# Kernel optimization log

Measured on AMD Instinct MI355X. Metric: run time of the kernel, lower is better.

## Reference

```python
import jax, jax.numpy as jnp
import numpy as np

NUM_BINS = 64


def _centers_width(num_bins):
    edges = np.linspace(-0.05, 1.05, num_bins + 1)
    delta = edges[2] - edges[1]
    centers = (edges + delta / 2)[:-1]
    return jnp.asarray(centers, jnp.float32), jnp.float32(delta / 2)

_CENTERS, _WIDTH = _centers_width(NUM_BINS)

_YUV = jnp.asarray([[0.299, 0.587, 0.114],
                    [-0.14713, -0.28886, 0.436],
                    [0.615, -0.51499, -0.10001]], jnp.float32)


def _soft_hist(img):
    # img: [B, C, H, W]; scale from [-1,1] -> [0,1] as in extract_hist
    img = (img + 1.0) * 0.5
    # bin_centers_conv (w=1, b=-center) -> x - c ; abs ; bin_widths_conv (w=-1, b=width) -> width - |x-c|
    d = jnp.abs(img[:, :, None, :, :] - _CENTERS[None, None, :, None, None])  # [B,C,bins,H,W]
    act = jnp.float32(1.01) ** (_WIDTH - d)
    act = jnp.where(act > 1.0, act, 0.0)  # nn.Threshold(1, 0)
    return act.mean(axis=(3, 4))  # AdaptiveAvgPool2d(1) -> [B, C, bins]


def _to_yuv(x):
    return jnp.einsum('ij,bjhw->bihw', _YUV, x)


def _emd(h1, h2):
    # per channel: mean over batch of sum over bins of cumsum diff; summed over channels
    diff = jnp.cumsum(h1, axis=-1) - jnp.cumsum(h2, axis=-1)  # [B,C,bins]
    return diff.sum(axis=-1).mean(axis=0).sum()


def setup_inputs() -> dict:
    key = jax.random.key(0)
    k1, k2 = jax.random.split(key)
    shape = (8, 3, 256, 256)
    return {
        'input_img': jax.random.normal(k1, shape, dtype=jnp.float32),
        'reference_img': jax.random.normal(k2, shape, dtype=jnp.float32),
    }


def reference(input_img, reference_img):
    total = _emd(_soft_hist(input_img), _soft_hist(reference_img))  # rgb
    total = total + _emd(_soft_hist(_to_yuv(input_img)), _soft_hist(_to_yuv(reference_img)))  # yuv
    return total
```

## Files before the change

kernel.cpp:

```cpp
#include <hip/hip_runtime.h>


#define HW    65536
#define BATCH 8
#define NPIX  (BATCH * HW)
#define BLOCK 256
#define NBLK  (NPIX / BLOCK)

__device__ __forceinline__ void channel_contrib(double v, double sign,
    const float* __restrict__ centers, double width, double L, double inv_step,
    double& aW, double& aE) {
  double u = (v + 1.0) * 0.5;
  double q = (u + 0.05) * inv_step;
  int kf = (int)floor(q);
  #pragma unroll
  for (int dk = -1; dk <= 1; ++dk) {
    int k = kf + dk;
    if ((unsigned)k < 64u) {
      double d = fabs(u - (double)centers[k]);
      double t = width - d;
      if (t > 0.0) {
        double z = L * t;
        double e = z * (1.0 + z * (0.5 + z * (1.0 / 6.0)));
        double w = (double)(64 - k);
        aW += sign * w;
        aE += sign * (w * e);
      }
    }
  }
}

__global__ __launch_bounds__(BLOCK) void hl_partial(
    const float* __restrict__ img_in, const float* __restrict__ img_ref,
    double* __restrict__ partials) {
  __shared__ float centers[64];
  __shared__ double red[8];

  const double start = -0.05;
  const double span  = 1.05 - (-0.05);
  const double step  = span / 64.0;
  const double e1    = 1.0 * step + start;
  const double e2    = 2.0 * step + start;
  const double halfw = (e2 - e1) * 0.5;
  const float  widthf = (float)halfw;
  if (threadIdx.x < 64) {
    double edge = (double)(int)threadIdx.x * step + start;
    centers[threadIdx.x] = (float)(edge + halfw);
  }
  __syncthreads();

  const double width = (double)widthf;
  const double L = log((double)1.01f);
  const double inv_step = 1.0 / step;

  double aW = 0.0, aE = 0.0;
  {
    int p  = blockIdx.x * BLOCK + threadIdx.x;
    int b  = p >> 16;
    int hw = p & (HW - 1);
    const float* pi = img_in  + (size_t)b * (3 * HW) + hw;
    const float* pr = img_ref + (size_t)b * (3 * HW) + hw;
    double r0 = (double)pi[0], g0 = (double)pi[HW], b0 = (double)pi[2 * HW];
    double r1 = (double)pr[0], g1 = (double)pr[HW], b1 = (double)pr[2 * HW];

    channel_contrib(r0,  1.0, centers, width, L, inv_step, aW, aE);
    channel_contrib(g0,  1.0, centers, width, L, inv_step, aW, aE);
    channel_contrib(b0,  1.0, centers, width, L, inv_step, aW, aE);
    channel_contrib(r1, -1.0, centers, width, L, inv_step, aW, aE);
    channel_contrib(g1, -1.0, centers, width, L, inv_step, aW, aE);
    channel_contrib(b1, -1.0, centers, width, L, inv_step, aW, aE);

    const double Y0 = (double)0.299f,    Y1 = (double)0.587f,    Y2 = (double)0.114f;
    const double U0 = (double)-0.14713f, U1 = (double)-0.28886f, U2 = (double)0.436f;
    const double V0 = (double)0.615f,    V1 = (double)-0.51499f, V2 = (double)-0.10001f;

    double yi = Y0 * r0 + Y1 * g0 + Y2 * b0;
    double ui = U0 * r0 + U1 * g0 + U2 * b0;
    double vi = V0 * r0 + V1 * g0 + V2 * b0;
    double yr = Y0 * r1 + Y1 * g1 + Y2 * b1;
    double ur = U0 * r1 + U1 * g1 + U2 * b1;
    double vr = V0 * r1 + V1 * g1 + V2 * b1;

    channel_contrib(yi,  1.0, centers, width, L, inv_step, aW, aE);
    channel_contrib(ui,  1.0, centers, width, L, inv_step, aW, aE);
    channel_contrib(vi,  1.0, centers, width, L, inv_step, aW, aE);
    channel_contrib(yr, -1.0, centers, width, L, inv_step, aW, aE);
    channel_contrib(ur, -1.0, centers, width, L, inv_step, aW, aE);
    channel_contrib(vr, -1.0, centers, width, L, inv_step, aW, aE);
  }

  #pragma unroll
  for (int off = 32; off > 0; off >>= 1) {
    aW += __shfl_down(aW, off);
    aE += __shfl_down(aE, off);
  }
  int wave = threadIdx.x >> 6;
  if ((threadIdx.x & 63) == 0) { red[wave * 2] = aW; red[wave * 2 + 1] = aE; }
  __syncthreads();

  if (threadIdx.x == 0) {
    double sW = 0.0, sE = 0.0;
    #pragma unroll
    for (int w = 0; w < 4; ++w) { sW += red[w * 2]; sE += red[w * 2 + 1]; }
    partials[2 * blockIdx.x]     = sW;
    partials[2 * blockIdx.x + 1] = sE;
  }
}

__global__ __launch_bounds__(BLOCK) void hl_final(
    const double* __restrict__ partials, float* __restrict__ out) {
  __shared__ double red[8];
  double sW = 0.0, sE = 0.0;
  for (int b = threadIdx.x; b < NBLK; b += BLOCK) {
    sW += partials[2 * b];
    sE += partials[2 * b + 1];
  }
  #pragma unroll
  for (int off = 32; off > 0; off >>= 1) {
    sW += __shfl_down(sW, off);
    sE += __shfl_down(sE, off);
  }
  int wave = threadIdx.x >> 6;
  if ((threadIdx.x & 63) == 0) { red[wave * 2] = sW; red[wave * 2 + 1] = sE; }
  __syncthreads();
  if (threadIdx.x == 0) {
    double tW = 0.0, tE = 0.0;
    #pragma unroll
    for (int w = 0; w < 4; ++w) { tW += red[w * 2]; tE += red[w * 2 + 1]; }
    out[0] = (float)((tW + tE) * (1.0 / (double)NPIX));
  }
}

extern "C" void kernel_launch(void* const* d_in, const int* in_sizes, int n_in,
                              void* d_out, int out_size, void* d_ws, size_t ws_size,
                              hipStream_t stream) {
  const float* img_in  = (const float*)d_in[0];
  const float* img_ref = (const float*)d_in[1];
  float* out = (float*)d_out;
  double* partials = (double*)d_ws;

  hl_partial<<<NBLK, BLOCK, 0, stream>>>(img_in, img_ref, partials);
  hl_final<<<1, BLOCK, 0, stream>>>(partials, out);
}
```

Measured before the change: 72.25 us.

## Move histogram contribution math to fp32 with int weights and two-bin search

The per-channel soft-histogram contribution drops from a three-bin scan to a two-bin candidate window computed in float. The exponential series is cut to second order in fp32, bin weights accumulate as integers, and sign handling is replaced by separate positive and negative accumulators. Each thread now processes two pixels, which halves the block count. These changes aim to cut the heavy fp64 ALU work, but the reduced precision and the truncated series could shift the result slightly.

```diff
diff --git a/kernel.cpp b/kernel.cpp
--- a/kernel.cpp
+++ b/kernel.cpp
@@ -2,29 +2,30 @@
 
 
 #define HW    65536
-#define BATCH 8
-#define NPIX  (BATCH * HW)
+#define NPIX  524288
 #define BLOCK 256
-#define NBLK  (NPIX / BLOCK)
+#define PXT   2
+#define NBLK  (NPIX / (BLOCK * PXT))
 
-__device__ __forceinline__ void channel_contrib(double v, double sign,
-    const float* __restrict__ centers, double width, double L, double inv_step,
-    double& aW, double& aE) {
+__device__ __forceinline__ void contrib(double v, float vf,
+    const float* __restrict__ centers, double width, float ga, float gb, float Lf,
+    int& aW, float& aE) {
+  float gg = fmaf(vf, ga, gb);
+  int k0 = (int)floorf(gg);
   double u = (v + 1.0) * 0.5;
-  double q = (u + 0.05) * inv_step;
-  int kf = (int)floor(q);
   #pragma unroll
-  for (int dk = -1; dk <= 1; ++dk) {
-    int k = kf + dk;
+  for (int dk = 0; dk <= 1; ++dk) {
+    int k = k0 + dk;
     if ((unsigned)k < 64u) {
-      double d = fabs(u - (double)centers[k]);
-      double t = width - d;
+      double d = u - (double)centers[k];
+      double t = width - fabs(d);
       if (t > 0.0) {
-        double z = L * t;
-        double e = z * (1.0 + z * (0.5 + z * (1.0 / 6.0)));
-        double w = (double)(64 - k);
-        aW += sign * w;
-        aE += sign * (w * e);
+        float tf = (float)t;
+        float z  = Lf * tf;
+        float e  = fmaf(0.5f * z, z, z);
+        int   w  = 64 - k;
+        aW += w;
+        aE  = fmaf((float)w, e, aE);
       }
     }
   }
@@ -34,11 +35,10 @@
     const float* __restrict__ img_in, const float* __restrict__ img_ref,
     double* __restrict__ partials) {
   __shared__ float centers[64];
-  __shared__ double red[8];
+  __shared__ double redW[4], redE[4];
 
   const double start = -0.05;
-  const double span  = 1.05 - (-0.05);
-  const double step  = span / 64.0;
+  const double step  = (1.05 - (-0.05)) / 64.0;
   const double e1    = 1.0 * step + start;
   const double e2    = 2.0 * step + start;
   const double halfw = (e2 - e1) * 0.5;
@@ -50,58 +50,66 @@
   __syncthreads();
 
   const double width = (double)widthf;
-  const double L = log((double)1.01f);
-  const double inv_step = 1.0 / step;
+  const float  Lf = (float)log((double)1.01f);
+  const float  ga = (float)(0.5 / step);
+  const float  gb = (float)(0.55 / step - 0.5);
 
-  double aW = 0.0, aE = 0.0;
-  {
-    int p  = blockIdx.x * BLOCK + threadIdx.x;
+  const double Y0 = (double)0.299f,    Y1 = (double)0.587f,    Y2 = (double)0.114f;
+  const double U0 = (double)-0.14713f, U1 = (double)-0.28886f, U2 = (double)0.436f;
+  const double V0 = (double)0.615f,    V1 = (double)-0.51499f, V2 = (double)-0.10001f;
+
+  int   aWp = 0,  aWn = 0;
+  float aEp = 0.f, aEn = 0.f;
+
+  const int base = blockIdx.x * (BLOCK * PXT) + threadIdx.x;
+  #pragma unroll
+  for (int i = 0; i < PXT; ++i) {
+    int p  = base + i * BLOCK;
     int b  = p >> 16;
     int hw = p & (HW - 1);
     const float* pi = img_in  + (size_t)b * (3 * HW) + hw;
     const float* pr = img_ref + (size_t)b * (3 * HW) + hw;
-    double r0 = (double)pi[0], g0 = (double)pi[HW], b0 = (double)pi[2 * HW];
-    double r1 = (double)pr[0], g1 = (double)pr[HW], b1 = (double)pr[2 * HW];
+    float r0 = pi[0], g0 = pi[HW], b0 = pi[2 * HW];
+    float r1 = pr[0], g1 = pr[HW], b1 = pr[2 * HW];
 
-    channel_contrib(r0,  1.0, centers, width, L, inv_step, aW, aE);
-    channel_contrib(g0,  1.0, centers, width, L, inv_step, aW, aE);
-    channel_contrib(b0,  1.0, centers, width, L, inv_step, aW, aE);
-    channel_contrib(r1, -1.0, centers, width, L, inv_step, aW, aE);
-    channel_contrib(g1, -1.0, centers, width, L, inv_step, aW, aE);
-    channel_contrib(b1, -1.0, centers, width, L, inv_step, aW, aE);
+    contrib((double)r0, r0, centers, width, ga, gb, Lf, aWp, aEp);
+    contrib((double)g0, g0, centers, width, ga, gb, Lf, aWp, aEp);
+    contrib((double)b0, b0, centers, width, ga, gb, Lf, aWp, aEp);
+    contrib((double)r1, r1, centers, width, ga, gb, Lf, aWn, aEn);
+    contrib((double)g1, g1, centers, width, ga, gb, Lf, aWn, aEn);
+    contrib((double)b1, b1, centers, width, ga, gb, Lf, aWn, aEn);
 
-    const double Y0 = (double)0.299f,    Y1 = (double)0.587f,    Y2 = (double)0.114f;
-    const double U0 = (double)-0.14713f, U1 = (double)-0.28886f, U2 = (double)0.436f;
-    const double V0 = (double)0.615f,    V1 = (double)-0.51499f, V2 = (double)-0.10001f;
+    double yi = fma(Y2, (double)b0, fma(Y1, (double)g0, Y0 * (double)r0));
+    double ui = fma(U2, (double)b0, fma(U1, (double)g0, U0 * (double)r0));
+    double vi = fma(V2, (double)b0, fma(V1, (double)g0, V0 * (double)r0));
+    double yr = fma(Y2, (double)b1, fma(Y1, (double)g1, Y0 * (double)r1));
+    double ur = fma(U2, (double)b1, fma(U1, (double)g1, U0 * (double)r1));
+    double vr = fma(V2, (double)b1, fma(V1, (double)g1, V0 * (double)r1));
 
-    double yi = Y0 * r0 + Y1 * g0 + Y2 * b0;
-    double ui = U0 * r0 + U1 * g0 + U2 * b0;
-    double vi = V0 * r0 + V1 * g0 + V2 * b0;
-    double yr = Y0 * r1 + Y1 * g1 + Y2 * b1;
-    double ur = U0 * r1 + U1 * g1 + U2 * b1;
-    double vr = V0 * r1 + V1 * g1 + V2 * b1;
+    contrib(yi, (float)yi, centers, width, ga, gb, Lf, aWp, aEp);
+    contrib(ui, (float)ui, centers, width, ga, gb, Lf, aWp, aEp);
+    contrib(vi, (float)vi, centers, width, ga, gb, Lf, aWp, aEp);
+    contrib(yr, (float)yr, centers, width, ga, gb, Lf, aWn, aEn);
+    contrib(ur, (float)ur, centers, width, ga, gb, Lf, aWn, aEn);
+    contrib(vr, (float)vr, centers, width, ga, gb, Lf, aWn, aEn);
+  }
 
-    channel_contrib(yi,  1.0, centers, width, L, inv_step, aW, aE);
-    channel_contrib(ui,  1.0, centers, width, L, inv_step, aW, aE);
-    channel_contrib(vi,  1.0, centers, width, L, inv_step, aW, aE);
-    channel_contrib(yr, -1.0, centers, width, L, inv_step, aW, aE);
-    channel_contrib(ur, -1.0, centers, width, L, inv_step, aW, aE);
-    channel_contrib(vr, -1.0, centers, width, L, inv_step, aW, aE);
-  }
+  int    aW = aWp - aWn;
+  double aE = (double)aEp - (double)aEn;
 
   #pragma unroll
   for (int off = 32; off > 0; off >>= 1) {
     aW += __shfl_down(aW, off);
     aE += __shfl_down(aE, off);
   }
-  int wave = threadIdx.x >> 6;
-  if ((threadIdx.x & 63) == 0) { red[wave * 2] = aW; red[wave * 2 + 1] = aE; }
+  int wv = threadIdx.x >> 6;
+  if ((threadIdx.x & 63) == 0) { redW[wv] = (double)aW; redE[wv] = aE; }
   __syncthreads();
 
   if (threadIdx.x == 0) {
     double sW = 0.0, sE = 0.0;
     #pragma unroll
-    for (int w = 0; w < 4; ++w) { sW += red[w * 2]; sE += red[w * 2 + 1]; }
+    for (int w = 0; w < 4; ++w) { sW += redW[w]; sE += redE[w]; }
     partials[2 * blockIdx.x]     = sW;
     partials[2 * blockIdx.x + 1] = sE;
   }
@@ -109,7 +117,7 @@
 
 __global__ __launch_bounds__(BLOCK) void hl_final(
     const double* __restrict__ partials, float* __restrict__ out) {
-  __shared__ double red[8];
+  __shared__ double redW[4], redE[4];
   double sW = 0.0, sE = 0.0;
   for (int b = threadIdx.x; b < NBLK; b += BLOCK) {
     sW += partials[2 * b];
@@ -120,13 +128,13 @@
     sW += __shfl_down(sW, off);
     sE += __shfl_down(sE, off);
   }
-  int wave = threadIdx.x >> 6;
-  if ((threadIdx.x & 63) == 0) { red[wave * 2] = sW; red[wave * 2 + 1] = sE; }
+  int wv = threadIdx.x >> 6;
+  if ((threadIdx.x & 63) == 0) { redW[wv] = sW; redE[wv] = sE; }
   __syncthreads();
   if (threadIdx.x == 0) {
     double tW = 0.0, tE = 0.0;
     #pragma unroll
-    for (int w = 0; w < 4; ++w) { tW += red[w * 2]; tE += red[w * 2 + 1]; }
+    for (int w = 0; w < 4; ++w) { tW += redW[w]; tE += redE[w]; }
     out[0] = (float)((tW + tE) * (1.0 / (double)NPIX));
   }
 }
```

New measurement: 69.61 us. 1.04x faster.
